# Kernel tuning notes

Measured on AMD Instinct MI355X. Metric: run time of the kernel, lower is better.

## Reference

```python
import jax, jax.numpy as jnp
import numpy as np

N = 50000
E = 800000
IN_C = 256
H1 = 64
H2 = 64
OUT_C = 32
HEADS = 7
NEG_SLOPE = 0.2


def _gat_layer(x, src, dst, W, a_src, a_dst, b, heads, ch, n_nodes):
    # x: [N, F_in]; W: [F_in, heads*ch]; a_src/a_dst: [heads, ch]; b: [heads*ch]
    h = (x @ W).reshape(n_nodes, heads, ch)                      # [N, H, C]
    alpha_s = jnp.einsum('nhc,hc->nh', h, a_src)                 # [N, H]
    alpha_d = jnp.einsum('nhc,hc->nh', h, a_dst)                 # [N, H]
    e = jax.nn.leaky_relu(alpha_s[src] + alpha_d[dst], NEG_SLOPE)  # [E, H]
    # segment softmax grouped by destination node
    m = jax.ops.segment_max(e, dst, num_segments=n_nodes)        # [N, H]
    e = jnp.exp(e - m[dst])
    denom = jax.ops.segment_sum(e, dst, num_segments=n_nodes)    # [N, H]
    alpha = e / (denom[dst] + 1e-16)                             # [E, H]
    msg = h[src] * alpha[:, :, None]                             # [E, H, C]
    out = jax.ops.segment_sum(msg, dst, num_segments=n_nodes)    # [N, H, C]
    return out.reshape(n_nodes, heads * ch) + b


def setup_inputs() -> dict:
    key = jax.random.key(0)
    ks = jax.random.split(key, 16)
    x = jax.random.normal(ks[0], (N, IN_C), dtype=jnp.float32)
    edge_index = jax.random.randint(ks[1], (2, E), 0, N, dtype=jnp.int32)

    def glorot(k, shape):
        fan = shape[0] + shape[-1]
        return jax.random.normal(k, shape, dtype=jnp.float32) * jnp.sqrt(2.0 / fan)

    W1 = glorot(ks[2], (IN_C, HEADS * H1))
    a1_src = glorot(ks[3], (HEADS, H1))
    a1_dst = glorot(ks[4], (HEADS, H1))
    b1 = jnp.zeros((HEADS * H1,), jnp.float32)

    W2 = glorot(ks[5], (HEADS * H1, HEADS * H2))
    a2_src = glorot(ks[6], (HEADS, H2))
    a2_dst = glorot(ks[7], (HEADS, H2))
    b2 = jnp.zeros((HEADS * H2,), jnp.float32)

    W3 = glorot(ks[8], (HEADS * H2, 1 * OUT_C))
    a3_src = glorot(ks[9], (1, OUT_C))
    a3_dst = glorot(ks[10], (1, OUT_C))
    b3 = jnp.zeros((OUT_C,), jnp.float32)

    return {"x": x, "edge_index": edge_index,
            "W1": W1, "a1_src": a1_src, "a1_dst": a1_dst, "b1": b1,
            "W2": W2, "a2_src": a2_src, "a2_dst": a2_dst, "b2": b2,
            "W3": W3, "a3_src": a3_src, "a3_dst": a3_dst, "b3": b3}


def reference(x, edge_index, W1, a1_src, a1_dst, b1, W2, a2_src, a2_dst, b2,
              W3, a3_src, a3_dst, b3):
    # PyG GATConv adds self-loops by default
    loops = jnp.arange(N, dtype=edge_index.dtype)
    src = jnp.concatenate([edge_index[0], loops])
    dst = jnp.concatenate([edge_index[1], loops])
    # dropout is identity in eval mode
    h = _gat_layer(x, src, dst, W1, a1_src, a1_dst, b1, HEADS, H1, N)
    h = jax.nn.relu(h)
    h = _gat_layer(h, src, dst, W2, a2_src, a2_dst, b2, HEADS, H2, N)
    h = jax.nn.relu(h)
    h = _gat_layer(h, src, dst, W3, a3_src, a3_dst, b3, 1, OUT_C, N)
    return jax.nn.log_softmax(h, axis=1)
```

## Files before the change

kernel.cpp:

```cpp
#include <hip/hip_runtime.h>
#include <hip/hip_bf16.h>
#include <hip/hip_fp16.h>

#define NN 50000
#define NP 50176
#define EE 800000
#define ET (EE + NN)
#define NB_SCAN ((NN + 255) / 256)

typedef __attribute__((ext_vector_type(8))) short bf16x8;
typedef __attribute__((ext_vector_type(4))) float f32x4;
typedef __attribute__((ext_vector_type(2))) float f32x2;
typedef __attribute__((ext_vector_type(4))) unsigned int u32x4;

static __device__ __forceinline__ float bf2f(__hip_bfloat16 x) { return __bfloat162float(x); }
static __device__ __forceinline__ ushort f2bu(float f) {
    union { __hip_bfloat16 b; ushort u; } c;
    c.b = __float2bfloat16(f);
    return c.u;
}
static __device__ __forceinline__ float u2f(ushort u) {
    union { ushort u; __hip_bfloat16 b; } c;
    c.u = u;
    return __bfloat162float(c.b);
}
static __device__ __forceinline__ unsigned char f2fp8(float v) {
    int p = __builtin_amdgcn_cvt_pk_fp8_f32(v, v, 0, false);
    return (unsigned char)(p & 0xff);
}
static __device__ __forceinline__ void fp8acc_pk(unsigned v, f32x2 w2, f32x2& a01, f32x2& a23) {
#if __has_builtin(__builtin_amdgcn_cvt_pk_f32_fp8)
    f32x2 f01 = __builtin_amdgcn_cvt_pk_f32_fp8((int)v, false);
    f32x2 f23 = __builtin_amdgcn_cvt_pk_f32_fp8((int)v, true);
#else
    f32x2 f01 = { __builtin_amdgcn_cvt_f32_fp8(v, 0), __builtin_amdgcn_cvt_f32_fp8(v, 1) };
    f32x2 f23 = { __builtin_amdgcn_cvt_f32_fp8(v, 2), __builtin_amdgcn_cvt_f32_fp8(v, 3) };
#endif
    asm("v_pk_fma_f32 %0, %1, %2, %0" : "+v"(a01) : "v"(f01), "v"(w2));
    asm("v_pk_fma_f32 %0, %1, %2, %0" : "+v"(a23) : "v"(f23), "v"(w2));
}
static __device__ __forceinline__ void gl2lds(const ushort* g, ushort* l) {
    __builtin_amdgcn_global_load_lds(
        (const __attribute__((address_space(1))) void*)g,
        (__attribute__((address_space(3))) void*)l,
        16, 0, 0);
}

#define PA1 (256 * 448)
#define PA2 (448 * 448)
#define PA3 (448 * 32)
#define PXQ (NN * 64)
#define PTOT (PA1 + PA2 + PA3 + PXQ)
#define PBLK ((PTOT + 255) / 256)
#define CBLK ((ET + 255) / 256)

__global__ void gat_prepcnt_kernel(const float* __restrict__ W1, const float* __restrict__ W2,
                                   const float* __restrict__ W3, const float* __restrict__ x,
                                   ushort* __restrict__ Wt1, ushort* __restrict__ Wt2,
                                   ushort* __restrict__ Wt3, ushort* __restrict__ xb,
                                   const int* __restrict__ ei, int* __restrict__ cnt) {
    int b = blockIdx.x;
    if (b >= PBLK) {
        int i = (b - PBLK) * 256 + threadIdx.x;
        if (i < ET) {
            int dst = (i < EE) ? ei[EE + i] : (i - EE);
            atomicAdd(&cnt[dst], 1);
        }
        return;
    }
    int i = b * 256 + threadIdx.x;
    if (i < PA1) {
        int k = i / 448, n = i - k * 448;
        Wt1[(size_t)n * 256 + k] = f2bu(W1[i]);
        return;
    }
    i -= PA1;
    if (i < PA2) {
        int k = i / 448, n = i - k * 448;
        Wt2[(size_t)n * 448 + k] = f2bu(W2[i]);
        return;
    }
    i -= PA2;
    if (i < PA3) {
        int k = i / 32, n = i - k * 32;
        Wt3[(size_t)n * 448 + k] = f2bu(W3[i]);
        return;
    }
    i -= PA3;
    if (i < PXQ) {
        float4 f = ((const float4*)x)[i];
        ushort u[4] = {f2bu(f.x), f2bu(f.y), f2bu(f.z), f2bu(f.w)};
        ((uint2*)xb)[i] = *(const uint2*)u;
    }
}

__global__ void gat_scan1_kernel(const int* __restrict__ cnt, int* __restrict__ tmp,
                                 int* __restrict__ part) {
    __shared__ int sm[256];
    int tid = threadIdx.x;
    int i = blockIdx.x * 256 + tid;
    int v = (i < NN) ? cnt[i] : 0;
    sm[tid] = v;
    __syncthreads();
    for (int o = 1; o < 256; o <<= 1) {
        int t = (tid >= o) ? sm[tid - o] : 0;
        __syncthreads();
        sm[tid] += t;
        __syncthreads();
    }
    if (i < NN) tmp[i] = sm[tid];
    if (tid == 255) part[blockIdx.x] = sm[255];
}

__global__ void gat_scan2_kernel(int* __restrict__ part) {
    __shared__ int sm[256];
    int tid = threadIdx.x;
    int v = (tid < NB_SCAN) ? part[tid] : 0;
    sm[tid] = v;
    __syncthreads();
    for (int o = 1; o < 256; o <<= 1) {
        int t = (tid >= o) ? sm[tid - o] : 0;
        __syncthreads();
        sm[tid] += t;
        __syncthreads();
    }
    part[tid] = sm[tid];
}

__global__ void gat_scan3_kernel(const int* __restrict__ tmp, const int* __restrict__ part,
                                 int* __restrict__ row_ptr) {
    int i = blockIdx.x * 256 + threadIdx.x;
    int off = (blockIdx.x > 0) ? part[blockIdx.x - 1] : 0;
    if (i < NN) row_ptr[i + 1] = tmp[i] + off;
    if (i == 0) row_ptr[0] = 0;
}

__global__ void gat_fill_kernel(const int* __restrict__ ei, const int* __restrict__ row_ptr,
                                int* __restrict__ fillc, int* __restrict__ colA) {
    int i = blockIdx.x * blockDim.x + threadIdx.x;
    if (i >= ET) return;
    int s, d;
    if (i < EE) { s = ei[i]; d = ei[EE + i]; }
    else        { s = d = i - EE; }
    int pos = row_ptr[d] + atomicAdd(&fillc[d], 1);
    colA[pos] = s;
}

#define GBN 64
#define GBK 32

template <int RF, int DOA, int OM>
__global__ __launch_bounds__(256) void gat_gemm_kernel(
    const ushort* __restrict__ A, const ushort* __restrict__ Wt,
    void* __restrict__ Cv,
    const float* __restrict__ Asrc, const float* __restrict__ Adst,
    float* __restrict__ as8, float* __restrict__ ad8,
    int M, int K, int N) {
    constexpr int GBM = RF * 64;
    constexpr int MT = NP / GBM;
    __shared__ __align__(16) ushort As[2][GBM * GBK];
    __shared__ __align__(16) ushort Bs[2][GBN * GBK];
    int tid = threadIdx.x;
    int wave = tid >> 6, lane = tid & 63;
    int lrow = lane & 15, lq = lane >> 4;

    int mt, head;
    if constexpr (DOA == 1) {
        int id = blockIdx.x;
        int xcd = id & 7, r = id >> 3;
        int g = r / 7;
        head = r - g * 7;
        mt = xcd + g * 8;
        if (mt >= MT) return;
    } else {
        mt = blockIdx.x;
        head = blockIdx.y;
    }
    int m0 = mt * GBM, n0 = head * GBN;

    int srow = lane >> 2, schunk = (lane & 3) * 8;
    f32x4 acc[RF][4] = {};

    int KT = K / GBK;
    {
#pragma unroll
        for (int q = 0; q < RF; q++) {
            const ushort* gp = A + (size_t)(m0 + wave * RF * 16 + q * 16 + srow) * K + schunk;
            gl2lds(gp, &As[0][(wave * RF * 16 + q * 16) * GBK]);
        }
        const ushort* gb = Wt + (size_t)(n0 + wave * 16 + srow) * K + schunk;
        gl2lds(gb, &Bs[0][wave * 16 * GBK]);
    }
    for (int kt = 0; kt < KT; kt++) {
        __syncthreads();
        if (kt + 1 < KT) {
            int nb = (kt + 1) & 1, k0 = (kt + 1) * GBK;
#pragma unroll
            for (int q = 0; q < RF; q++) {
                const ushort* gp = A + (size_t)(m0 + wave * RF * 16 + q * 16 + srow) * K + k0 + schunk;
                gl2lds(gp, &As[nb][(wave * RF * 16 + q * 16) * GBK]);
            }
            const ushort* gb = Wt + (size_t)(n0 + wave * 16 + srow) * K + k0 + schunk;
            gl2lds(gb, &Bs[nb][wave * 16 * GBK]);
        }
        int b = kt & 1;
        bf16x8 af[RF];
#pragma unroll
        for (int rf = 0; rf < RF; rf++)
            af[rf] = *(const bf16x8*)&As[b][(wave * RF * 16 + rf * 16 + lrow) * GBK + lq * 8];
#pragma unroll
        for (int ng = 0; ng < 4; ng++) {
            bf16x8 bf = *(const bf16x8*)&Bs[b][(ng * 16 + lrow) * GBK + lq * 8];
#pragma unroll
            for (int rf = 0; rf < RF; rf++)
                acc[rf][ng] = __builtin_amdgcn_mfma_f32_16x16x32_bf16(af[rf], bf, acc[rf][ng], 0, 0, 0);
        }
    }
#pragma unroll
    for (int rf = 0; rf < RF; rf++)
#pragma unroll
        for (int ng = 0; ng < 4; ng++)
#pragma unroll
            for (int r = 0; r < 4; r++) {
                int row = m0 + wave * RF * 16 + rf * 16 + lq * 4 + r;
                int colI = n0 + ng * 16 + lrow;
                if (row < M && colI < N) {
                    if constexpr (OM == 0)
                        ((__hip_bfloat16*)Cv)[(size_t)row * N + colI] = __float2bfloat16(acc[rf][ng][r]);
                    else
                        ((unsigned char*)Cv)[(size_t)row * N + colI] = f2fp8(acc[rf][ng][r]);
                }
            }
    if constexpr (DOA == 1) {
        float as_l[4], ad_l[4];
#pragma unroll
        for (int ng = 0; ng < 4; ng++) {
            as_l[ng] = Asrc[head * 64 + ng * 16 + lrow];
            ad_l[ng] = Adst[head * 64 + ng * 16 + lrow];
        }
#pragma unroll
        for (int rf = 0; rf < RF; rf++)
#pragma unroll
            for (int r = 0; r < 4; r++) {
                float ps = 0.f, pd = 0.f;
#pragma unroll
                for (int ng = 0; ng < 4; ng++) {
                    ps += acc[rf][ng][r] * as_l[ng];
                    pd += acc[rf][ng][r] * ad_l[ng];
                }
#pragma unroll
                for (int o = 1; o < 16; o <<= 1) {
                    ps += __shfl_xor(ps, o);
                    pd += __shfl_xor(pd, o);
                }
                int row = m0 + wave * RF * 16 + rf * 16 + lq * 4 + r;
                if (lrow == 0 && row < M) {
                    as8[(size_t)row * 8 + head] = ps;
                    ad8[(size_t)row * 8 + head] = pd;
                }
            }
    } else if constexpr (DOA == 2) {
        float as_l[2], ad_l[2];
#pragma unroll
        for (int ng = 0; ng < 2; ng++) {
            as_l[ng] = Asrc[ng * 16 + lrow];
            ad_l[ng] = Adst[ng * 16 + lrow];
        }
#pragma unroll
        for (int rf = 0; rf < RF; rf++)
#pragma unroll
            for (int r = 0; r < 4; r++) {
                float ps = acc[rf][0][r] * as_l[0] + acc[rf][1][r] * as_l[1];
                float pd = acc[rf][0][r] * ad_l[0] + acc[rf][1][r] * ad_l[1];
#pragma unroll
                for (int o = 1; o < 16; o <<= 1) {
                    ps += __shfl_xor(ps, o);
                    pd += __shfl_xor(pd, o);
                }
                int row = m0 + wave * RF * 16 + rf * 16 + lq * 4 + r;
                if (lrow == 0 && row < M) {
                    as8[(size_t)row * 8] = ps;
                    ad8[(size_t)row * 8] = pd;
                }
            }
    }
}

__global__ void gat_aggC7_kernel(const int* __restrict__ rp, const int* __restrict__ colA,
                                 const float* __restrict__ as8, const float* __restrict__ ad8,
                                 const unsigned char* __restrict__ h8,
                                 const float* __restrict__ bias,
                                 __hip_bfloat16* __restrict__ outp) {
    int d = blockIdx.x * 4 + (threadIdx.x >> 6);
    if (d >= NN) return;
    int lane = threadIdx.x & 63;
    int lc = (lane < 56) ? lane : 55;
    unsigned hh = (unsigned)(lc >> 3);
    unsigned lb = (unsigned)lc * 8u;
    float adh = ad8[(size_t)d * 8 + hh];
    int s0 = rp[d], s1 = rp[d + 1];
    int s1m1 = s1 - 1;
    f32x2 a01 = {0.f, 0.f}, a23 = {0.f, 0.f}, a45 = {0.f, 0.f}, a67 = {0.f, 0.f};
    float den = 0.f;

#define GATHER4(B4, ASV, HV) do {                                      \
        _Pragma("unroll")                                              \
        for (int k_ = 0; k_ < 4; k_++) {                               \
            unsigned s_ = (unsigned)__builtin_amdgcn_readlane(myIdx, (B4) + k_); \
            ASV[k_] = as8[s_ * 8u + hh];                               \
            HV[k_] = *(const uint2*)(h8 + (s_ * 448u + lb));           \
        }                                                              \
    } while (0)

#define CONSUME(ASV, HV, JJ) do {                                      \
        float w_[4];                                                   \
        _Pragma("unroll")                                              \
        for (int k_ = 0; k_ < 4; k_++) {                               \
            float e_ = ASV[k_] + adh;                                  \
            e_ = (e_ > 0.f) ? e_ : 0.2f * e_;                          \
            float ww_ = __expf(e_);                                    \
            ww_ = ((JJ) + k_ < s1) ? ww_ : 0.f;                        \
            w_[k_] = ww_;                                              \
            den += ww_;                                                \
        }                                                              \
        _Pragma("unroll")                                              \
        for (int k_ = 0; k_ < 4; k_++) {                               \
            f32x2 w2_ = {w_[k_], w_[k_]};                              \
            fp8acc_pk(HV[k_].x, w2_, a01, a23);                        \
            fp8acc_pk(HV[k_].y, w2_, a45, a67);                        \
        }                                                              \
    } while (0)

    for (int base = s0; base < s1; base += 64) {
        int myIdx = __builtin_nontemporal_load(colA + (unsigned)min(base + lane, s1m1));
        int cnt = min(s1 - base, 64);
        int nb = (cnt + 3) >> 2;
        int jb = base;
        int b4 = 0;
        float as0v[4], as1v[4];
        uint2 hv0[4], hv1[4];
        GATHER4(0, as0v, hv0);
        int rem = nb - 1;
        while (rem >= 2) {
            GATHER4(b4 + 4, as1v, hv1); CONSUME(as0v, hv0, jb); jb += 4;
            GATHER4(b4 + 8, as0v, hv0); CONSUME(as1v, hv1, jb); jb += 4;
            b4 += 8; rem -= 2;
        }
        if (rem == 1) {
            GATHER4(b4 + 4, as1v, hv1); CONSUME(as0v, hv0, jb); jb += 4;
            CONSUME(as1v, hv1, jb);
        } else {
            CONSUME(as0v, hv0, jb);
        }
    }
#undef GATHER4
#undef CONSUME

    float inv = 1.f / (den + 1e-16f);
    const float4* bp = (const float4*)(bias + lb);
    float4 bb0 = bp[0], bb1 = bp[1];
    float bv[8] = {bb0.x, bb0.y, bb0.z, bb0.w, bb1.x, bb1.y, bb1.z, bb1.w};
    float av[8] = {a01.x, a01.y, a23.x, a23.y, a45.x, a45.y, a67.x, a67.y};
    ushort o8[8];
#pragma unroll
    for (int k = 0; k < 8; k++) {
        float o = av[k] * inv + bv[k];
        o = fmaxf(o, 0.f);
        o8[k] = f2bu(o);
    }
    if (lane < 56) {
        u32x4 ov = *(const u32x4*)o8;
        __builtin_nontemporal_store(ov, (u32x4*)((ushort*)outp + (size_t)d * 448 + lane * 8));
    }
}

__global__ void gat_aggCF_kernel(const int* __restrict__ rp, const int* __restrict__ colA,
                                 const float* __restrict__ as8, const float* __restrict__ ad8,
                                 const __hip_bfloat16* __restrict__ h,
                                 const float* __restrict__ bias,
                                 float* __restrict__ outp) {
    int wid = blockIdx.x * 4 + (threadIdx.x >> 6);
    int lane = threadIdx.x & 63;
    int half = lane >> 5;
    unsigned c = (unsigned)(lane & 31);
    int dreal = wid * 2 + half;
    bool valid = dreal < NN;
    int d = valid ? dreal : (NN - 1);
    float adh = ad8[(size_t)d * 8];
    int s0 = rp[d], s1 = rp[d + 1];
    float acc = 0.f, den = 0.f;
    int j = s0;
    for (; j + 2 <= s1; j += 2) {
        unsigned ju = (unsigned)j;
        unsigned sA = (unsigned)__builtin_nontemporal_load(colA + ju);
        unsigned sB = (unsigned)__builtin_nontemporal_load(colA + ju + 1);
        float eA = as8[sA * 8u] + adh;
        float eB = as8[sB * 8u] + adh;
        float vA = bf2f(h[sA * 32u + c]);
        float vB = bf2f(h[sB * 32u + c]);
        eA = (eA > 0.f) ? eA : 0.2f * eA;
        eB = (eB > 0.f) ? eB : 0.2f * eB;
        float wA = __expf(eA), wB = __expf(eB);
        den += wA + wB;
        acc += wA * vA + wB * vB;
    }
    for (; j < s1; j++) {
        unsigned s = (unsigned)__builtin_nontemporal_load(colA + (unsigned)j);
        float e = as8[s * 8u] + adh;
        e = (e > 0.f) ? e : 0.2f * e;
        float w = __expf(e);
        den += w;
        acc += w * bf2f(h[s * 32u + c]);
    }
    float o = acc / (den + 1e-16f) + bias[c];
    float t = o;
#pragma unroll
    for (int off = 16; off > 0; off >>= 1) t = fmaxf(t, __shfl_xor(t, off));
    float ex = __expf(o - t);
#pragma unroll
    for (int off = 16; off > 0; off >>= 1) ex += __shfl_xor(ex, off);
    float res = o - t - __logf(ex);
    if (valid) __builtin_nontemporal_store(res, &outp[(size_t)d * 32 + c]);
}

extern "C" void kernel_launch(void* const* d_in, const int* in_sizes, int n_in,
                              void* d_out, int out_size, void* d_ws, size_t ws_size,
                              hipStream_t stream) {
    const float* x   = (const float*)d_in[0];
    const int*   ei  = (const int*)d_in[1];
    const float* W1  = (const float*)d_in[2];
    const float* a1s = (const float*)d_in[3];
    const float* a1d = (const float*)d_in[4];
    const float* b1  = (const float*)d_in[5];
    const float* W2  = (const float*)d_in[6];
    const float* a2s = (const float*)d_in[7];
    const float* a2d = (const float*)d_in[8];
    const float* b2  = (const float*)d_in[9];
    const float* W3  = (const float*)d_in[10];
    const float* a3s = (const float*)d_in[11];
    const float* a3d = (const float*)d_in[12];
    const float* b3  = (const float*)d_in[13];
    float* out = (float*)d_out;

    char* w = (char*)d_ws;
    unsigned char* hbuf8 = (unsigned char*)w;
    __hip_bfloat16* hbuf3 = (__hip_bfloat16*)w;
    ushort* xb = (ushort*)(w + (size_t)NP * 448);
    __hip_bfloat16* act = (__hip_bfloat16*)(xb + (size_t)NP * 256);
    float* as8 = (float*)(act + (size_t)NP * 448);
    float* ad8 = as8 + (size_t)NN * 8;
    int* cnt     = (int*)(ad8 + (size_t)NN * 8);
    int* fillc   = cnt + NN;
    int* row_ptr = fillc + NN;
    int* tmp     = row_ptr + (NN + 4);
    int* part    = tmp + NN;
    int* colA    = part + 256;
    char* pw = (char*)(colA + ET);
    pw = (char*)(((uintptr_t)pw + 15) & ~(uintptr_t)15);
    ushort* Wt1 = (ushort*)pw;
    ushort* Wt2 = Wt1 + 448 * 256;
    ushort* Wt3 = Wt2 + 448 * 448;

    hipMemsetAsync(cnt, 0, 2 * (size_t)NN * sizeof(int), stream);

    gat_prepcnt_kernel<<<PBLK + CBLK, 256, 0, stream>>>(W1, W2, W3, x, Wt1, Wt2, Wt3, xb, ei, cnt);
    gat_scan1_kernel<<<NB_SCAN, 256, 0, stream>>>(cnt, tmp, part);
    gat_scan2_kernel<<<1, 256, 0, stream>>>(part);
    gat_scan3_kernel<<<NB_SCAN, 256, 0, stream>>>(tmp, part, row_ptr);
    gat_fill_kernel<<<CBLK, 256, 0, stream>>>(ei, row_ptr, fillc, colA);

    dim3 gemmBlk(256);
    int swzBlocks = 8 * ((196 + 7) / 8) * 7;
    int mtiles1 = NP / 64;
    int aggBlocks = (NN + 3) / 4;

    gat_gemm_kernel<4, 1, 1><<<swzBlocks, gemmBlk, 0, stream>>>(
        xb, Wt1, hbuf8, a1s, a1d, as8, ad8, NN, 256, 448);
    gat_aggC7_kernel<<<aggBlocks, 256, 0, stream>>>(row_ptr, colA, as8, ad8, hbuf8, b1, act);

    gat_gemm_kernel<4, 1, 1><<<swzBlocks, gemmBlk, 0, stream>>>(
        (const ushort*)act, Wt2, hbuf8, a2s, a2d, as8, ad8, NN, 448, 448);
    gat_aggC7_kernel<<<aggBlocks, 256, 0, stream>>>(row_ptr, colA, as8, ad8, hbuf8, b2, act);

    gat_gemm_kernel<1, 2, 0><<<dim3(mtiles1, 1), gemmBlk, 0, stream>>>(
        (const ushort*)act, Wt3, hbuf3, a3s, a3d, as8, ad8, NN, 448, 32);
    int fBlocks = (NN + 7) / 8;
    gat_aggCF_kernel<<<fBlocks, 256, 0, stream>>>(row_ptr, colA, as8, ad8, hbuf3, b3, out);
}
```

Measured before the change: 481.1 us.

## Compute attention weights per edge group once and deepen gather pipeline to 8

In the 7-head aggregation kernel, each lane now computes the leaky-relu/exp attention weight for one (head, edge) pair across eight edge groups up front. The weights are broadcast with shuffles during accumulation, so each weight is no longer recomputed redundantly by all eight lanes of a head. The fp8 feature gather is restructured into 8-edge double-buffered batches with guarded issue/consume steps. This reduces redundant exp work and scalar as8 loads and increases memory-level parallelism, at the cost of more registers, shuffle traffic, and full-batch work for low-degree nodes.

```diff
diff --git a/kernel.cpp b/kernel.cpp
--- a/kernel.cpp
+++ b/kernel.cpp
@@ -297,63 +297,64 @@
     int lc = (lane < 56) ? lane : 55;
     unsigned hh = (unsigned)(lc >> 3);
     unsigned lb = (unsigned)lc * 8u;
+    int j8 = lane & 7;
+    int gsel = lane & 56;
     float adh = ad8[(size_t)d * 8 + hh];
     int s0 = rp[d], s1 = rp[d + 1];
     int s1m1 = s1 - 1;
     f32x2 a01 = {0.f, 0.f}, a23 = {0.f, 0.f}, a45 = {0.f, 0.f}, a67 = {0.f, 0.f};
     float den = 0.f;
 
-#define GATHER4(B4, ASV, HV) do {                                      \
+#define ISSUE(T, BUF) do {                                             \
         _Pragma("unroll")                                              \
-        for (int k_ = 0; k_ < 4; k_++) {                               \
-            unsigned s_ = (unsigned)__builtin_amdgcn_readlane(myIdx, (B4) + k_); \
-            ASV[k_] = as8[s_ * 8u + hh];                               \
-            HV[k_] = *(const uint2*)(h8 + (s_ * 448u + lb));           \
+        for (int k2_ = 0; k2_ < 8; k2_++) {                            \
+            unsigned s_ = (unsigned)__builtin_amdgcn_readlane(myIdx, (T) * 8 + k2_); \
+            BUF[k2_] = *(const uint2*)(h8 + (s_ * 448u + lb));         \
         }                                                              \
     } while (0)
 
-#define CONSUME(ASV, HV, JJ) do {                                      \
-        float w_[4];                                                   \
+#define CONSUME(T, BUF) do {                                           \
         _Pragma("unroll")                                              \
-        for (int k_ = 0; k_ < 4; k_++) {                               \
-            float e_ = ASV[k_] + adh;                                  \
-            e_ = (e_ > 0.f) ? e_ : 0.2f * e_;                          \
-            float ww_ = __expf(e_);                                    \
-            ww_ = ((JJ) + k_ < s1) ? ww_ : 0.f;                        \
-            w_[k_] = ww_;                                              \
-            den += ww_;                                                \
-        }                                                              \
-        _Pragma("unroll")                                              \
-        for (int k_ = 0; k_ < 4; k_++) {                               \
-            f32x2 w2_ = {w_[k_], w_[k_]};                              \
-            fp8acc_pk(HV[k_].x, w2_, a01, a23);                        \
-            fp8acc_pk(HV[k_].y, w2_, a45, a67);                        \
+        for (int k2_ = 0; k2_ < 8; k2_++) {                            \
+            float w_ = __shfl(wv[T], gsel | k2_);                      \
+            den += w_;                                                 \
+            f32x2 w2_ = {w_, w_};                                      \
+            fp8acc_pk(BUF[k2_].x, w2_, a01, a23);                      \
+            fp8acc_pk(BUF[k2_].y, w2_, a45, a67);                      \
         }                                                              \
     } while (0)
 
     for (int base = s0; base < s1; base += 64) {
         int myIdx = __builtin_nontemporal_load(colA + (unsigned)min(base + lane, s1m1));
-        int cnt = min(s1 - base, 64);
-        int nb = (cnt + 3) >> 2;
-        int jb = base;
-        int b4 = 0;
-        float as0v[4], as1v[4];
-        uint2 hv0[4], hv1[4];
-        GATHER4(0, as0v, hv0);
-        int rem = nb - 1;
-        while (rem >= 2) {
-            GATHER4(b4 + 4, as1v, hv1); CONSUME(as0v, hv0, jb); jb += 4;
-            GATHER4(b4 + 8, as0v, hv0); CONSUME(as1v, hv1, jb); jb += 4;
-            b4 += 8; rem -= 2;
-        }
-        if (rem == 1) {
-            GATHER4(b4 + 4, as1v, hv1); CONSUME(as0v, hv0, jb); jb += 4;
-            CONSUME(as1v, hv1, jb);
-        } else {
-            CONSUME(as0v, hv0, jb);
-        }
-    }
-#undef GATHER4
+        float wv[8];
+#pragma unroll
+        for (int t = 0; t < 8; t++) {
+            int e = j8 + 8 * t;
+            unsigned s_ = (unsigned)__shfl(myIdx, e);
+            float ev = as8[s_ * 8u + hh] + adh;
+            ev = (ev > 0.f) ? ev : 0.2f * ev;
+            float w = __expf(ev);
+            wv[t] = (base + e < s1) ? w : 0.f;
+        }
+        uint2 hva[8], hvb[8];
+        ISSUE(0, hva);
+        if (base +  8 < s1) ISSUE(1, hvb);
+        CONSUME(0, hva);
+        if (base + 16 < s1) ISSUE(2, hva);
+        if (base +  8 < s1) CONSUME(1, hvb);
+        if (base + 24 < s1) ISSUE(3, hvb);
+        if (base + 16 < s1) CONSUME(2, hva);
+        if (base + 32 < s1) ISSUE(4, hva);
+        if (base + 24 < s1) CONSUME(3, hvb);
+        if (base + 40 < s1) ISSUE(5, hvb);
+        if (base + 32 < s1) CONSUME(4, hva);
+        if (base + 48 < s1) ISSUE(6, hva);
+        if (base + 40 < s1) CONSUME(5, hvb);
+        if (base + 56 < s1) ISSUE(7, hvb);
+        if (base + 48 < s1) CONSUME(6, hva);
+        if (base + 56 < s1) CONSUME(7, hvb);
+    }
+#undef ISSUE
 #undef CONSUME
 
     float inv = 1.f / (den + 1e-16f);
```

After: 484.6 us. Within noise of the previous version (+0.7%).

## Use full-width 64x448 GEMM tile so each A row-block is loaded once

Applied to the files above, without the earlier changes.

Replaces the per-head 256x64 tiled GEMM (with XCD swizzle) for layers 1 and 2 with a new kernel in which each block computes a 64-row by 448-column tile covering all 7 heads. The A tile is read once per row-block instead of once per head, which cuts global traffic for the activations. The cost is 112 accumulator registers per lane and about 64KB of LDS for the double-buffered B tile, which lowers occupancy, and each A fragment is reused across 28 MFMAs per k-step. The XCD swizzle and the DOA==1 branch are removed from the generic kernel.

```diff
diff --git a/kernel.cpp b/kernel.cpp
--- a/kernel.cpp
+++ b/kernel.cpp
@@ -146,6 +146,94 @@
     colA[pos] = s;
 }
 
+__global__ __launch_bounds__(256) void gat_gemmF_kernel(
+    const ushort* __restrict__ A, const ushort* __restrict__ Wt,
+    unsigned char* __restrict__ C8,
+    const float* __restrict__ Asrc, const float* __restrict__ Adst,
+    float* __restrict__ as8, float* __restrict__ ad8,
+    int K) {
+    __shared__ __align__(16) ushort As[2][64 * 32];
+    __shared__ __align__(16) ushort Bs[2][448 * 32];
+    int tid = threadIdx.x;
+    int wave = tid >> 6, lane = tid & 63;
+    int lrow = lane & 15, lq = lane >> 4;
+    int m0 = blockIdx.x * 64;
+    int srow = lane >> 2, schunk = (lane & 3) * 8;
+    f32x4 acc[7][4] = {};
+
+    int KT = K / 32;
+    {
+        const ushort* gp = A + (size_t)(m0 + wave * 16 + srow) * K + schunk;
+        gl2lds(gp, &As[0][(wave * 16) * 32]);
+#pragma unroll
+        for (int q = 0; q < 7; q++) {
+            const ushort* gb = Wt + (size_t)(wave * 112 + q * 16 + srow) * K + schunk;
+            gl2lds(gb, &Bs[0][(wave * 112 + q * 16) * 32]);
+        }
+    }
+    for (int kt = 0; kt < KT; kt++) {
+        __syncthreads();
+        if (kt + 1 < KT) {
+            int nb = (kt + 1) & 1, k0 = (kt + 1) * 32;
+            const ushort* gp = A + (size_t)(m0 + wave * 16 + srow) * K + k0 + schunk;
+            gl2lds(gp, &As[nb][(wave * 16) * 32]);
+#pragma unroll
+            for (int q = 0; q < 7; q++) {
+                const ushort* gb = Wt + (size_t)(wave * 112 + q * 16 + srow) * K + k0 + schunk;
+                gl2lds(gb, &Bs[nb][(wave * 112 + q * 16) * 32]);
+            }
+        }
+        int b = kt & 1;
+        bf16x8 af = *(const bf16x8*)&As[b][(wave * 16 + lrow) * 32 + lq * 8];
+#pragma unroll
+        for (int h = 0; h < 7; h++)
+#pragma unroll
+            for (int ng = 0; ng < 4; ng++) {
+                bf16x8 bf = *(const bf16x8*)&Bs[b][(h * 64 + ng * 16 + lrow) * 32 + lq * 8];
+                acc[h][ng] = __builtin_amdgcn_mfma_f32_16x16x32_bf16(af, bf, acc[h][ng], 0, 0, 0);
+            }
+    }
+#pragma unroll
+    for (int h = 0; h < 7; h++)
+#pragma unroll
+        for (int ng = 0; ng < 4; ng++)
+#pragma unroll
+            for (int r = 0; r < 4; r++) {
+                int row = m0 + wave * 16 + lq * 4 + r;
+                int col = h * 64 + ng * 16 + lrow;
+                if (row < NN)
+                    C8[(size_t)row * 448 + col] = f2fp8(acc[h][ng][r]);
+            }
+#pragma unroll
+    for (int h = 0; h < 7; h++) {
+        float as_l[4], ad_l[4];
+#pragma unroll
+        for (int ng = 0; ng < 4; ng++) {
+            as_l[ng] = Asrc[h * 64 + ng * 16 + lrow];
+            ad_l[ng] = Adst[h * 64 + ng * 16 + lrow];
+        }
+#pragma unroll
+        for (int r = 0; r < 4; r++) {
+            float ps = 0.f, pd = 0.f;
+#pragma unroll
+            for (int ng = 0; ng < 4; ng++) {
+                ps += acc[h][ng][r] * as_l[ng];
+                pd += acc[h][ng][r] * ad_l[ng];
+            }
+#pragma unroll
+            for (int o = 1; o < 16; o <<= 1) {
+                ps += __shfl_xor(ps, o);
+                pd += __shfl_xor(pd, o);
+            }
+            int row = m0 + wave * 16 + lq * 4 + r;
+            if (lrow == 0 && row < NN) {
+                as8[(size_t)row * 8 + h] = ps;
+                ad8[(size_t)row * 8 + h] = pd;
+            }
+        }
+    }
+}
+
 #define GBN 64
 #define GBK 32
 
@@ -157,25 +245,12 @@
     float* __restrict__ as8, float* __restrict__ ad8,
     int M, int K, int N) {
     constexpr int GBM = RF * 64;
-    constexpr int MT = NP / GBM;
     __shared__ __align__(16) ushort As[2][GBM * GBK];
     __shared__ __align__(16) ushort Bs[2][GBN * GBK];
     int tid = threadIdx.x;
     int wave = tid >> 6, lane = tid & 63;
     int lrow = lane & 15, lq = lane >> 4;
-
-    int mt, head;
-    if constexpr (DOA == 1) {
-        int id = blockIdx.x;
-        int xcd = id & 7, r = id >> 3;
-        int g = r / 7;
-        head = r - g * 7;
-        mt = xcd + g * 8;
-        if (mt >= MT) return;
-    } else {
-        mt = blockIdx.x;
-        head = blockIdx.y;
-    }
+    int mt = blockIdx.x, head = blockIdx.y;
     int m0 = mt * GBM, n0 = head * GBN;
 
     int srow = lane >> 2, schunk = (lane & 3) * 8;
@@ -231,35 +306,7 @@
                         ((unsigned char*)Cv)[(size_t)row * N + colI] = f2fp8(acc[rf][ng][r]);
                 }
             }
-    if constexpr (DOA == 1) {
-        float as_l[4], ad_l[4];
-#pragma unroll
-        for (int ng = 0; ng < 4; ng++) {
-            as_l[ng] = Asrc[head * 64 + ng * 16 + lrow];
-            ad_l[ng] = Adst[head * 64 + ng * 16 + lrow];
-        }
-#pragma unroll
-        for (int rf = 0; rf < RF; rf++)
-#pragma unroll
-            for (int r = 0; r < 4; r++) {
-                float ps = 0.f, pd = 0.f;
-#pragma unroll
-                for (int ng = 0; ng < 4; ng++) {
-                    ps += acc[rf][ng][r] * as_l[ng];
-                    pd += acc[rf][ng][r] * ad_l[ng];
-                }
-#pragma unroll
-                for (int o = 1; o < 16; o <<= 1) {
-                    ps += __shfl_xor(ps, o);
-                    pd += __shfl_xor(pd, o);
-                }
-                int row = m0 + wave * RF * 16 + rf * 16 + lq * 4 + r;
-                if (lrow == 0 && row < M) {
-                    as8[(size_t)row * 8 + head] = ps;
-                    ad8[(size_t)row * 8 + head] = pd;
-                }
-            }
-    } else if constexpr (DOA == 2) {
+    if constexpr (DOA == 2) {
         float as_l[2], ad_l[2];
 #pragma unroll
         for (int ng = 0; ng < 2; ng++) {
@@ -470,19 +517,18 @@
     gat_fill_kernel<<<CBLK, 256, 0, stream>>>(ei, row_ptr, fillc, colA);
 
     dim3 gemmBlk(256);
-    int swzBlocks = 8 * ((196 + 7) / 8) * 7;
-    int mtiles1 = NP / 64;
+    int mtilesF = NP / 64;
     int aggBlocks = (NN + 3) / 4;
 
-    gat_gemm_kernel<4, 1, 1><<<swzBlocks, gemmBlk, 0, stream>>>(
-        xb, Wt1, hbuf8, a1s, a1d, as8, ad8, NN, 256, 448);
+    gat_gemmF_kernel<<<mtilesF, gemmBlk, 0, stream>>>(
+        xb, Wt1, hbuf8, a1s, a1d, as8, ad8, 256);
     gat_aggC7_kernel<<<aggBlocks, 256, 0, stream>>>(row_ptr, colA, as8, ad8, hbuf8, b1, act);
 
-    gat_gemm_kernel<4, 1, 1><<<swzBlocks, gemmBlk, 0, stream>>>(
-        (const ushort*)act, Wt2, hbuf8, a2s, a2d, as8, ad8, NN, 448, 448);
+    gat_gemmF_kernel<<<mtilesF, gemmBlk, 0, stream>>>(
+        (const ushort*)act, Wt2, hbuf8, a2s, a2d, as8, ad8, 448);
     gat_aggC7_kernel<<<aggBlocks, 256, 0, stream>>>(row_ptr, colA, as8, ad8, hbuf8, b2, act);
 
-    gat_gemm_kernel<1, 2, 0><<<dim3(mtiles1, 1), gemmBlk, 0, stream>>>(
+    gat_gemm_kernel<1, 2, 0><<<dim3(mtilesF, 1), gemmBlk, 0, stream>>>(
         (const ushort*)act, Wt3, hbuf3, a3s, a3d, as8, ad8, NN, 448, 32);
     int fBlocks = (NN + 7) / 8;
     gat_aggCF_kernel<<<fBlocks, 256, 0, stream>>>(row_ptr, colA, as8, ad8, hbuf3, b3, out);
```

Result: slower. 514.7 us (+7.0%).
